# Optimization experiments

Measured on AMD Instinct MI355X. Metric: run time of the kernel, lower is better.

The kernel has to match this reference:

```python
import jax, jax.numpy as jnp
import numpy as np
import math

EMBED_DIMS = 256
NUM_LANDMARKS = 40  # hard-coded k=40 in the original module
B, N = 2, 8192


def setup_inputs() -> dict:
    key = jax.random.key(0)
    ks = jax.random.split(key, 9)
    C = EMBED_DIMS
    w = lambda k: jax.random.normal(k, (C, C), dtype=jnp.float32) * 0.02
    b = lambda k: jax.random.normal(k, (C,), dtype=jnp.float32) * 0.02
    return {
        "query": jax.random.normal(ks[0], (B, N, C), dtype=jnp.float32),
        "Wq": w(ks[1]), "bq": b(ks[2]),
        "Wk": w(ks[3]), "bk": b(ks[4]),
        "Wv": w(ks[5]), "bv": b(ks[6]),
        "Wo": w(ks[7]), "bo": b(ks[8]),
    }


def reference(query, Wq, bq, Wk, bk, Wv, bv, Wo, bo):
    # key = value = identity = query (defaults in the original forward)
    C = query.shape[-1]
    scaling = math.sqrt(C)

    q = query @ Wq.T + bq  # [B, N, C]
    k = query @ Wk.T + bk
    v = query @ Wv.T + bv

    # Full similarity only to score keys: score_m[b, m] = sum_n sim_nm[b, n, m]
    sim_nm = jnp.einsum('bnc,bmc->bnm', q, k) / scaling  # [B, N, N]
    score_m = sim_nm.sum(axis=1)                          # [B, N]

    _, top_idx = jax.lax.top_k(score_m, NUM_LANDMARKS)    # [B, 40]
    selected = jnp.take_along_axis(k, top_idx[:, :, None], axis=1)  # [B, 40, C]

    sim_qn = jax.nn.softmax(jnp.einsum('bnc,bkc->bnk', q, selected) / scaling, axis=-1)  # [B, N, 40]
    sim_km = jax.nn.softmax(jnp.einsum('bmc,bkc->bmk', k, selected) / scaling, axis=-1)  # [B, N, 40]

    sim_qk = jnp.einsum('bnk,bmk->bnm', sim_qn, sim_km)   # [B, N, N]
    out = jnp.einsum('bnm,bmc->bnc', sim_qk, v)           # [B, N, C]
    out = out @ Wo.T + bo
    return query + out  # identity residual; dropouts are identity at p=0
```

## Files before the change

kernel.cpp:

```cpp
#include <hip/hip_runtime.h>
#include <cstddef>
#include <cstdint>

#define BATCH 2
#define SEQ 8192
#define CH 256
#define NLM 40
#define NLMP 48
#define MROWS (BATCH * SEQ)
#define INV_SCALE 0.0625f
#define NCBLK 256

typedef unsigned short ushort_t;
typedef __attribute__((ext_vector_type(8))) short short8;
typedef __attribute__((ext_vector_type(4))) float floatx4;

__device__ __forceinline__ ushort_t f2bf(float f) {
    unsigned int u = __float_as_uint(f);
    u += 0x7FFFu + ((u >> 16) & 1u);
    return (ushort_t)(u >> 16);
}
__device__ __forceinline__ float bf2f(ushort_t u) {
    return __uint_as_float(((unsigned)u) << 16);
}

__device__ __forceinline__ void gload_lds16(const ushort_t* g, ushort_t* l) {
    __builtin_amdgcn_global_load_lds(
        (const __attribute__((address_space(1))) unsigned int*)g,
        (__attribute__((address_space(3))) unsigned int*)l, 16, 0, 0);
}

__global__ __launch_bounds__(256) void convert_colsum(const float* __restrict__ x,
                                                      ushort_t* __restrict__ xbf,
                                                      float* __restrict__ partial) {
    __shared__ float red[4][256];
    const int b = blockIdx.y;
    const int r0 = blockIdx.x * 32;
    const int t = threadIdx.x;
    const int c4 = (t & 63) * 4;
    const int rg = t >> 6;
    const float* base = x + ((size_t)b * SEQ + r0) * 256;
    ushort_t* obase = xbf + ((size_t)b * SEQ + r0) * 256;
    float4 s = {0.f, 0.f, 0.f, 0.f};
#pragma unroll
    for (int i = 0; i < 8; i++) {
        const int r = rg + i * 4;
        const float4 a = *(const float4*)&base[(size_t)r * 256 + c4];
        uint2 o;
        o.x = f2bf(a.x) | ((unsigned)f2bf(a.y) << 16);
        o.y = f2bf(a.z) | ((unsigned)f2bf(a.w) << 16);
        *(uint2*)&obase[(size_t)r * 256 + c4] = o;
        s.x += a.x; s.y += a.y; s.z += a.z; s.w += a.w;
    }
    *(float4*)&red[rg][c4] = s;
    __syncthreads();
    const float tot = red[0][t] + red[1][t] + red[2][t] + red[3][t];
    partial[((size_t)b * NCBLK + blockIdx.x) * 256 + t] = tot;
}

__global__ __launch_bounds__(1024) void ws_kernel(const float* __restrict__ partial,
                                                  const float* __restrict__ Wq,
                                                  const float* __restrict__ bq,
                                                  const float* __restrict__ Wk,
                                                  float* __restrict__ ws,
                                                  float* __restrict__ tmat) {
    const int b = blockIdx.x;
    __shared__ float xs[256];
    __shared__ float qs[256];
    __shared__ float ppart[4][256];
    const int t = threadIdx.x;
    {
        float* tz = tmat + (size_t)b * NLM * 256;
        for (int i = t; i < NLM * 256; i += 1024) tz[i] = 0.f;
    }
    {
        const int c = t & 255, qd = t >> 8;
        const float* pb = partial + ((size_t)b * NCBLK + qd * 64) * 256 + c;
        float a = 0.f;
#pragma unroll 8
        for (int i = 0; i < 64; i++) a += pb[(size_t)i * 256];
        ppart[qd][c] = a;
    }
    __syncthreads();
    if (t < 256) xs[t] = ppart[0][t] + ppart[1][t] + ppart[2][t] + ppart[3][t];
    __syncthreads();
    const int lane = t & 63, w = t >> 6;
    {
        float4 wq[16];
#pragma unroll
        for (int g = 0; g < 16; g++)
            wq[g] = *(const float4*)&Wq[(size_t)(w * 16 + g) * 256 + lane * 4];
        const float4 x4 = *(const float4*)&xs[lane * 4];
#pragma unroll
        for (int g = 0; g < 16; g++) {
            const int o = w * 16 + g;
            float d = wq[g].x * x4.x + wq[g].y * x4.y + wq[g].z * x4.z + wq[g].w * x4.w;
#pragma unroll
            for (int off = 32; off >= 1; off >>= 1) d += __shfl_down(d, off);
            if (lane == 0) qs[o] = d + 8192.0f * bq[o];
        }
    }
    __syncthreads();
    const int c = t & 255, part = t >> 8;
    float a = 0.f;
#pragma unroll 16
    for (int o = part * 64; o < part * 64 + 64; o++)
        a += Wk[(size_t)o * 256 + c] * qs[o];
    ppart[part][c] = a;
    __syncthreads();
    if (t < 256)
        ws[b * 256 + t] = ppart[0][t] + ppart[1][t] + ppart[2][t] + ppart[3][t];
}

__global__ __launch_bounds__(256) void gemm_qkv_score(const ushort_t* __restrict__ xbf,
                                                      const float* __restrict__ Wq,
                                                      const float* __restrict__ Wk,
                                                      const float* __restrict__ Wv,
                                                      const float* __restrict__ bq,
                                                      const float* __restrict__ bk,
                                                      const float* __restrict__ bv,
                                                      ushort_t* __restrict__ qkv,
                                                      const float* __restrict__ query,
                                                      const float* __restrict__ ws,
                                                      float* __restrict__ score) {
    __shared__ __align__(16) char smem[24576];
    ushort_t* As = (ushort_t*)smem;
    ushort_t* Bs = (ushort_t*)(smem + 16384);
    ushort_t* Es = (ushort_t*)smem;
    const int lin = blockIdx.x;
    const int wg = (lin & 7) * 256 + (lin >> 3);
    const int bx = wg & 3;
    const int by = (wg >> 2) & 127;
    const int z = wg >> 9;
    const int t = threadIdx.x;
    const int lane = t & 63;
    const int w = t >> 6;

    if (z == 3) {
        const int blk = by * 4 + bx;
#pragma unroll
        for (int i = 0; i < 8; i++) {
            const int g = blk * 32 + i * 4 + w;
            const int b = g >> 13;
            const int m = g & 8191;
            const float4 kv = *(const float4*)&query[(size_t)g * 256 + lane * 4];
            const float4 qs = *(const float4*)&ws[b * 256 + lane * 4];
            float d = kv.x * qs.x + kv.y * qs.y + kv.z * qs.z + kv.w * qs.w;
#pragma unroll
            for (int off = 32; off >= 1; off >>= 1) d += __shfl_down(d, off);
            if (lane == 0) score[(size_t)b * SEQ + m] = d * INV_SCALE;
        }
        return;
    }

    const float* __restrict__ W = (z == 0) ? Wq : (z == 1) ? Wk : Wv;
    const float* __restrict__ bias = (z == 0) ? bq : (z == 1) ? bk : bv;
    ushort_t* __restrict__ out = qkv + (size_t)z * MROWS * 256;
    const int o0 = bx * 64;
    const int m0 = by * 128;
    const int quad = lane >> 4;
    const int l16 = lane & 15;
    const int xsw = l16 & 7;

    floatx4 acc[2][4];
#pragma unroll
    for (int rt = 0; rt < 2; rt++)
#pragma unroll
        for (int ct = 0; ct < 4; ct++) acc[rt][ct] = (floatx4){0.f, 0.f, 0.f, 0.f};

    for (int kc = 0; kc < 256; kc += 64) {
#pragma unroll
        for (int q = 0; q < 4; q++) {
            const int r0 = w * 32 + q * 8;
            gload_lds16(&xbf[(size_t)(m0 + r0 + (lane >> 3)) * 256 + kc +
                             (((lane & 7) ^ (lane >> 3)) * 8)],
                        &As[r0 * 64]);
        }
#pragma unroll
        for (int u = 0; u < 2; u++) {
            const int cid = t + u * 256;
            const int row = cid >> 3;
            const int cch = cid & 7;
            const float* wp = &W[(size_t)(o0 + row) * 256 + kc + cch * 8];
            const float4 a = *(const float4*)wp;
            const float4 c = *(const float4*)(wp + 4);
            uint4 o;
            o.x = f2bf(a.x) | ((unsigned)f2bf(a.y) << 16);
            o.y = f2bf(a.z) | ((unsigned)f2bf(a.w) << 16);
            o.z = f2bf(c.x) | ((unsigned)f2bf(c.y) << 16);
            o.w = f2bf(c.z) | ((unsigned)f2bf(c.w) << 16);
            *(uint4*)&Bs[row * 64 + ((cch ^ (row & 7)) * 8)] = o;
        }
        __syncthreads();
#pragma unroll
        for (int s = 0; s < 2; s++) {
            short8 a[2], bf[4];
#pragma unroll
            for (int rt = 0; rt < 2; rt++)
                a[rt] = *(const short8*)&As[(w * 32 + rt * 16 + l16) * 64 +
                                            (((s * 4 + quad) ^ xsw) * 8)];
#pragma unroll
            for (int ct = 0; ct < 4; ct++)
                bf[ct] = *(const short8*)&Bs[(ct * 16 + l16) * 64 +
                                             (((s * 4 + quad) ^ xsw) * 8)];
#pragma unroll
            for (int rt = 0; rt < 2; rt++)
#pragma unroll
                for (int ct = 0; ct < 4; ct++)
                    acc[rt][ct] = __builtin_amdgcn_mfma_f32_16x16x32_bf16(
                        a[rt], bf[ct], acc[rt][ct], 0, 0, 0);
        }
        __syncthreads();
    }

#pragma unroll
    for (int rt = 0; rt < 2; rt++) {
#pragma unroll
        for (int ct = 0; ct < 4; ct++) {
            const int col = ct * 16 + l16;
            const float bb = bias[o0 + col];
#pragma unroll
            for (int reg = 0; reg < 4; reg++) {
                const int row = w * 32 + rt * 16 + quad * 4 + reg;
                Es[row * 72 + col] = f2bf(acc[rt][ct][reg] + bb);
            }
        }
    }
    __syncthreads();
#pragma unroll
    for (int u = 0; u < 4; u++) {
        const int cid = t + u * 256;
        const int row = cid >> 3;
        const int off = (cid & 7) * 8;
        *(uint4*)&out[(size_t)(m0 + row) * 256 + o0 + off] =
            *(const uint4*)&Es[row * 72 + off];
    }
}

__global__ __launch_bounds__(1024) void topk_gather(const float* __restrict__ score,
                                                    const ushort_t* __restrict__ kmat,
                                                    ushort_t* __restrict__ sel) {
    const int b = blockIdx.x;
    const int t = threadIdx.x;
    __shared__ unsigned hist[256];
    __shared__ unsigned wsum[64];
    __shared__ unsigned sPrefix, sMask, sRem, sNeq;
    __shared__ int sNgt;
    __shared__ int top[NLM];
    __shared__ unsigned topkey[NLM];

    unsigned key[8];
#pragma unroll
    for (int j = 0; j < 8; j++) {
        const unsigned u = __float_as_uint(score[(size_t)b * SEQ + t + j * 1024]);
        key[j] = u ^ (unsigned)(((int)u >> 31) | 0x80000000);
    }
    if (t == 0) { sPrefix = 0; sMask = 0; sRem = NLM; sNgt = 0; sNeq = 0; }

    for (int lvl = 0; lvl < 4; lvl++) {
        const int shift = 24 - 8 * lvl;
        if (t < 256) hist[t] = 0;
        __syncthreads();
        const unsigned pfx = sPrefix, msk = sMask;
#pragma unroll
        for (int j = 0; j < 8; j++)
            if (((key[j] ^ pfx) & msk) == 0)
                atomicAdd(&hist[(key[j] >> shift) & 255u], 1u);
        __syncthreads();
        if (t < 64) wsum[t] = hist[t * 4] + hist[t * 4 + 1] + hist[t * 4 + 2] + hist[t * 4 + 3];
        __syncthreads();
        if (t == 0) {
            unsigned rem = sRem, cum = 0;
            int g = 63;
            for (; g > 0; g--) { if (cum + wsum[g] >= rem) break; cum += wsum[g]; }
            int d = g * 4 + 3;
            for (; d > g * 4; d--) { if (cum + hist[d] >= rem) break; cum += hist[d]; }
            sRem = rem - cum;
            sPrefix |= ((unsigned)d) << shift;
            sMask |= 255u << shift;
        }
        __syncthreads();
    }
    const unsigned K40 = sPrefix;
    const unsigned rem = sRem;
    const int ngt = NLM - (int)rem;

#pragma unroll
    for (int j = 0; j < 8; j++) {
        if (key[j] > K40) {
            const int slot = atomicAdd(&sNgt, 1);
            top[slot] = t + j * 1024; topkey[slot] = key[j];
        } else if (key[j] == K40) {
            const unsigned e = atomicAdd(&sNeq, 1u);
            if (e < rem) {
                const int slot = ngt + (int)e;
                top[slot] = t + j * 1024; topkey[slot] = key[j];
            }
        }
    }
    __syncthreads();

    if (t < 64) {
        unsigned long long c = (t < NLM)
            ? ((((unsigned long long)(~topkey[t])) << 32) | (unsigned)top[t])
            : 0xFFFFFFFFFFFFFFFFull;
#pragma unroll
        for (int kk = 2; kk <= 64; kk <<= 1) {
#pragma unroll
            for (int j = kk >> 1; j >= 1; j >>= 1) {
                const unsigned long long o = __shfl_xor(c, j);
                const bool takeMin = ((t & kk) == 0) == ((t & j) == 0);
                const bool less = c < o;
                c = (takeMin == less) ? c : o;
            }
        }
        if (t < NLM) top[t] = (int)(c & 0xFFFFFFFFu);
    }
    __syncthreads();

    for (int f = t; f < NLMP * 256; f += 1024) {
        const int j = f >> 8;
        const int cc = f & 255;
        sel[(size_t)b * NLMP * 256 + f] =
            (j < NLM) ? kmat[((size_t)b * SEQ + top[j]) * 256 + cc] : (ushort_t)0;
    }
}

__global__ __launch_bounds__(256, 4) void sim_fused(const ushort_t* __restrict__ qbf,
                                                    const ushort_t* __restrict__ kbf,
                                                    const ushort_t* __restrict__ vbf,
                                                    const ushort_t* __restrict__ sel,
                                                    float* __restrict__ simq,
                                                    float* __restrict__ tmat) {
    __shared__ __align__(16) char smem[43008];
    float (*Ps)[40]  = (float(*)[40])smem;
    ushort_t* Vs     = (ushort_t*)(smem + 10240);
    const int b = blockIdx.y;
    const int n0 = blockIdx.x * 64;
    const int t = threadIdx.x;
    const int lane = t & 63;
    const int w = t >> 6;
    const int quad = lane >> 4;
    const int l16 = lane & 15;
    const ushort_t* __restrict__ A = (blockIdx.z == 0) ? qbf : kbf;
    const ushort_t* __restrict__ Arow = A + ((size_t)b * SEQ + n0 + w * 16 + l16) * 256;
    const ushort_t* __restrict__ Sb = sel + (size_t)b * NLMP * 256 + (size_t)l16 * 256;

    floatx4 acc[3];
#pragma unroll
    for (int ct = 0; ct < 3; ct++) acc[ct] = (floatx4){0.f, 0.f, 0.f, 0.f};

#pragma unroll
    for (int ks = 0; ks < 8; ks++) {
        const int ko = ks * 32 + quad * 8;
        const short8 a  = *(const short8*)&Arow[ko];
        const short8 b0 = *(const short8*)&Sb[ko];
        const short8 b1 = *(const short8*)&Sb[16 * 256 + ko];
        const short8 b2 = *(const short8*)&Sb[32 * 256 + ko];
        acc[0] = __builtin_amdgcn_mfma_f32_16x16x32_bf16(a, b0, acc[0], 0, 0, 0);
        acc[1] = __builtin_amdgcn_mfma_f32_16x16x32_bf16(a, b1, acc[1], 0, 0, 0);
        acc[2] = __builtin_amdgcn_mfma_f32_16x16x32_bf16(a, b2, acc[2], 0, 0, 0);
    }

    const bool v2ok = (l16 < 8);
    float p0[4], p1[4], p2[4];
#pragma unroll
    for (int reg = 0; reg < 4; reg++) {
        const float l0 = acc[0][reg] * INV_SCALE;
        const float l1 = acc[1][reg] * INV_SCALE;
        const float l2 = acc[2][reg] * INV_SCALE;
        float m = fmaxf(l0, l1);
        if (v2ok) m = fmaxf(m, l2);
        m = fmaxf(m, __shfl_xor(m, 1));
        m = fmaxf(m, __shfl_xor(m, 2));
        m = fmaxf(m, __shfl_xor(m, 4));
        m = fmaxf(m, __shfl_xor(m, 8));
        const float e0 = expf(l0 - m);
        const float e1 = expf(l1 - m);
        const float e2 = v2ok ? expf(l2 - m) : 0.f;
        float s = e0 + e1 + e2;
        s += __shfl_xor(s, 1);
        s += __shfl_xor(s, 2);
        s += __shfl_xor(s, 4);
        s += __shfl_xor(s, 8);
        const float inv = 1.f / s;
        p0[reg] = e0 * inv; p1[reg] = e1 * inv; p2[reg] = e2 * inv;
    }

    const int row0 = w * 16 + quad * 4;
    if (blockIdx.z == 0) {
        float* __restrict__ dst = &simq[((size_t)b * SEQ + n0 + row0) * NLM];
#pragma unroll
        for (int reg = 0; reg < 4; reg++) {
            float* __restrict__ d2 = dst + reg * NLM;
            d2[l16] = p0[reg];
            d2[16 + l16] = p1[reg];
            if (v2ok) d2[32 + l16] = p2[reg];
        }
        return;
    }

#pragma unroll
    for (int reg = 0; reg < 4; reg++) {
        Ps[row0 + reg][l16] = p0[reg];
        Ps[row0 + reg][16 + l16] = p1[reg];
        if (v2ok) Ps[row0 + reg][32 + l16] = p2[reg];
    }
#pragma unroll
    for (int u = 0; u < 8; u++) {
        gload_lds16(&vbf[((size_t)b * SEQ + n0 + w * 2 + u * 8 + (lane >> 5)) * 256 +
                         (lane & 31) * 8],
                    &Vs[(w * 2 + u * 8) * 256]);
    }
    __syncthreads();

    float tac[40];
#pragma unroll
    for (int j = 0; j < 40; j++) tac[j] = 0.f;

#pragma unroll 2
    for (int m = 0; m < 64; m++) {
        const float vv = bf2f(Vs[m * 256 + t]);
#pragma unroll
        for (int j4 = 0; j4 < 10; j4++) {
            const float4 p = *(const float4*)&Ps[m][j4 * 4];
            tac[j4 * 4 + 0] = fmaf(p.x, vv, tac[j4 * 4 + 0]);
            tac[j4 * 4 + 1] = fmaf(p.y, vv, tac[j4 * 4 + 1]);
            tac[j4 * 4 + 2] = fmaf(p.z, vv, tac[j4 * 4 + 2]);
            tac[j4 * 4 + 3] = fmaf(p.w, vv, tac[j4 * 4 + 3]);
        }
    }
#pragma unroll
    for (int j = 0; j < 40; j++)
        atomicAdd(&tmat[(size_t)b * NLM * 256 + j * 256 + t], tac[j]);
}

__global__ __launch_bounds__(512) void out_fused(const float* __restrict__ simq,
                                                 const float* __restrict__ tmat,
                                                 const float* __restrict__ Wo,
                                                 const float* __restrict__ bias,
                                                 const float* __restrict__ resid,
                                                 float* __restrict__ out) {
    __shared__ __align__(16) char smem[51200];
    float* Ps = (float*)smem;
    ushort_t* Ac = (ushort_t*)(smem + 10240);
    ushort_t* Bs = (ushort_t*)(smem + 18432);

    const int t = threadIdx.x;
    const int m0 = blockIdx.x * 64;
    const int b = blockIdx.x >> 7;
    const int lane = t & 63;
    const int w = t >> 6;
    const int quad = lane >> 4;
    const int l16 = lane & 15;
    const int xsw = l16 & 7;
    const int rt_base = (w & 3) * 16;
    const int cg_base = (w >> 2) * 8;

    for (int f = t; f < 64 * NLM; f += 512)
        Ps[f] = simq[(size_t)m0 * NLM + f];
    __syncthreads();

    floatx4 acc[8];
#pragma unroll
    for (int ct = 0; ct < 8; ct++) acc[ct] = (floatx4){0.f, 0.f, 0.f, 0.f};

    const int kl = t & 63;
    const int rg = t >> 6;
    const float* __restrict__ Tb = tmat + (size_t)b * NLM * 256;

    for (int kc = 0; kc < 256; kc += 64) {
        {
            float tc[40];
#pragma unroll
            for (int l = 0; l < 40; l++) tc[l] = Tb[l * 256 + kc + kl];
#pragma unroll
            for (int r = rg * 8; r < rg * 8 + 8; r++) {
                float a = 0.f;
#pragma unroll
                for (int j4 = 0; j4 < 10; j4++) {
                    const float4 p = *(const float4*)&Ps[r * 40 + j4 * 4];
                    a = fmaf(p.x, tc[j4 * 4 + 0], a);
                    a = fmaf(p.y, tc[j4 * 4 + 1], a);
                    a = fmaf(p.z, tc[j4 * 4 + 2], a);
                    a = fmaf(p.w, tc[j4 * 4 + 3], a);
                }
                Ac[r * 64 + (((kl >> 3) ^ (r & 7)) * 8) + (kl & 7)] = f2bf(a);
            }
        }
#pragma unroll
        for (int u = 0; u < 4; u++) {
            const int cid = t + u * 512;
            const int row = cid >> 3;
            const int cch = cid & 7;
            const float* wp = &Wo[(size_t)row * 256 + kc + cch * 8];
            const float4 a = *(const float4*)wp;
            const float4 c = *(const float4*)(wp + 4);
            uint4 o;
            o.x = f2bf(a.x) | ((unsigned)f2bf(a.y) << 16);
            o.y = f2bf(a.z) | ((unsigned)f2bf(a.w) << 16);
            o.z = f2bf(c.x) | ((unsigned)f2bf(c.y) << 16);
            o.w = f2bf(c.z) | ((unsigned)f2bf(c.w) << 16);
            *(uint4*)&Bs[row * 64 + ((cch ^ (row & 7)) * 8)] = o;
        }
        __syncthreads();
#pragma unroll
        for (int s = 0; s < 2; s++) {
            const short8 a = *(const short8*)&Ac[(rt_base + l16) * 64 +
                                                 (((s * 4 + quad) ^ xsw) * 8)];
#pragma unroll
            for (int ct = 0; ct < 8; ct++) {
                const short8 bf = *(const short8*)&Bs[((cg_base + ct) * 16 + l16) * 64 +
                                                      (((s * 4 + quad) ^ xsw) * 8)];
                acc[ct] = __builtin_amdgcn_mfma_f32_16x16x32_bf16(a, bf, acc[ct], 0, 0, 0);
            }
        }
        __syncthreads();
    }

#pragma unroll
    for (int ct = 0; ct < 8; ct++) {
        const int col = (cg_base + ct) * 16 + l16;
        const float bb = bias[col];
#pragma unroll
        for (int reg = 0; reg < 4; reg++) {
            const int row = rt_base + quad * 4 + reg;
            const size_t idx = (size_t)(m0 + row) * 256 + col;
            out[idx] = (acc[ct][reg] + bb) + resid[idx];
        }
    }
}

extern "C" void kernel_launch(void* const* d_in, const int* in_sizes, int n_in,
                              void* d_out, int out_size, void* d_ws, size_t ws_size,
                              hipStream_t stream) {
    const float* query = (const float*)d_in[0];
    const float* Wq = (const float*)d_in[1];
    const float* bq = (const float*)d_in[2];
    const float* Wk = (const float*)d_in[3];
    const float* bk = (const float*)d_in[4];
    const float* Wv = (const float*)d_in[5];
    const float* bv = (const float*)d_in[6];
    const float* Wo = (const float*)d_in[7];
    const float* bo = (const float*)d_in[8];
    float* out = (float*)d_out;

    char* p = (char*)d_ws;
    float* simq  = (float*)p;            p += (size_t)MROWS * NLM * 4;
    ushort_t* selbf = (ushort_t*)p;      p += (size_t)BATCH * NLMP * 256 * 2;
    float* tmat  = (float*)p;            p += (size_t)BATCH * NLM * 256 * 4;
    float* partial = (float*)p;          p += (size_t)BATCH * NCBLK * 256 * 4;
    float* ws    = (float*)p;            p += (size_t)BATCH * 256 * 4;
    float* score = (float*)p;            p += (size_t)BATCH * SEQ * 4;
    ushort_t* qkv = (ushort_t*)p;        p += (size_t)3 * MROWS * 256 * 2;
    ushort_t* xbf = (ushort_t*)p;        p += (size_t)MROWS * 256 * 2;
    ushort_t* qbf = qkv;
    ushort_t* kbf = qkv + (size_t)MROWS * 256;
    ushort_t* vbf = qkv + (size_t)2 * MROWS * 256;

    const dim3 blk(256);

    convert_colsum<<<dim3(SEQ / 32, BATCH), blk, 0, stream>>>(query, xbf, partial);
    ws_kernel<<<dim3(BATCH), dim3(1024), 0, stream>>>(partial, Wq, bq, Wk, ws, tmat);

    gemm_qkv_score<<<dim3(2048), blk, 0, stream>>>(
        xbf, Wq, Wk, Wv, bq, bk, bv, qkv, query, ws, score);

    topk_gather<<<dim3(BATCH), dim3(1024), 0, stream>>>(score, kbf, selbf);

    sim_fused<<<dim3(SEQ / 64, BATCH, 2), blk, 0, stream>>>(qbf, kbf, vbf, selbf, simq, tmat);

    out_fused<<<dim3(MROWS / 64), dim3(512), 0, stream>>>(simq, tmat, Wo, bo, query, out);
}
```

Measured before the change: 185.2 us.

## Precompute full P·T tile once in out_fused and parallelize top-k digit search

Result: faster. 175.3 us, median of 2 (-5.3%).

```diff
diff --git a/kernel.cpp b/kernel.cpp
--- a/kernel.cpp
+++ b/kernel.cpp
@@ -243,7 +243,6 @@
     const int b = blockIdx.x;
     const int t = threadIdx.x;
     __shared__ unsigned hist[256];
-    __shared__ unsigned wsum[64];
     __shared__ unsigned sPrefix, sMask, sRem, sNeq;
     __shared__ int sNgt;
     __shared__ int top[NLM];
@@ -267,17 +266,26 @@
             if (((key[j] ^ pfx) & msk) == 0)
                 atomicAdd(&hist[(key[j] >> shift) & 255u], 1u);
         __syncthreads();
-        if (t < 64) wsum[t] = hist[t * 4] + hist[t * 4 + 1] + hist[t * 4 + 2] + hist[t * 4 + 3];
-        __syncthreads();
-        if (t == 0) {
-            unsigned rem = sRem, cum = 0;
-            int g = 63;
-            for (; g > 0; g--) { if (cum + wsum[g] >= rem) break; cum += wsum[g]; }
-            int d = g * 4 + 3;
-            for (; d > g * 4; d--) { if (cum + hist[d] >= rem) break; cum += hist[d]; }
-            sRem = rem - cum;
-            sPrefix |= ((unsigned)d) << shift;
-            sMask |= 255u << shift;
+        if (t < 64) {
+            unsigned sfx = hist[t * 4] + hist[t * 4 + 1] + hist[t * 4 + 2] + hist[t * 4 + 3];
+#pragma unroll
+            for (int off = 1; off < 64; off <<= 1) {
+                const unsigned o = __shfl_down(sfx, off);
+                if (t + off < 64) sfx += o;
+            }
+            const unsigned rem = sRem;
+            const unsigned long long mk = __ballot(sfx >= rem);
+            const int gstar = 63 - __builtin_clzll(mk);
+            unsigned S1 = __shfl(sfx, (gstar + 1) & 63);
+            if (gstar == 63) S1 = 0u;
+            if (t == 0) {
+                int d = gstar * 4 + 3;
+                unsigned cum = S1;
+                for (; d > gstar * 4; d--) { if (cum + hist[d] >= rem) break; cum += hist[d]; }
+                sRem = rem - cum;
+                sPrefix |= ((unsigned)d) << shift;
+                sMask |= 255u << shift;
+            }
         }
         __syncthreads();
     }
@@ -441,10 +449,10 @@
                                                  const float* __restrict__ bias,
                                                  const float* __restrict__ resid,
                                                  float* __restrict__ out) {
-    __shared__ __align__(16) char smem[51200];
+    __shared__ __align__(16) char smem[75776];
     float* Ps = (float*)smem;
     ushort_t* Ac = (ushort_t*)(smem + 10240);
-    ushort_t* Bs = (ushort_t*)(smem + 18432);
+    ushort_t* Bs = (ushort_t*)(smem + 43008);
 
     const int t = threadIdx.x;
     const int m0 = blockIdx.x * 64;
@@ -461,33 +469,36 @@
         Ps[f] = simq[(size_t)m0 * NLM + f];
     __syncthreads();
 
+    {
+        const int col = t & 255;
+        const int r0 = (t >> 8) * 32;
+        const float* __restrict__ Tb = tmat + (size_t)b * NLM * 256;
+        float tc[40];
+#pragma unroll
+        for (int l = 0; l < 40; l++) tc[l] = Tb[l * 256 + col];
+        const int chunk = col >> 3;
+#pragma unroll
+        for (int r = 0; r < 32; r++) {
+            const int rr = r0 + r;
+            float a = 0.f;
+#pragma unroll
+            for (int j4 = 0; j4 < 10; j4++) {
+                const float4 p = *(const float4*)&Ps[rr * 40 + j4 * 4];
+                a = fmaf(p.x, tc[j4 * 4 + 0], a);
+                a = fmaf(p.y, tc[j4 * 4 + 1], a);
+                a = fmaf(p.z, tc[j4 * 4 + 2], a);
+                a = fmaf(p.w, tc[j4 * 4 + 3], a);
+            }
+            const int pch = (chunk & ~7) | ((chunk & 7) ^ (rr & 7));
+            Ac[rr * 256 + pch * 8 + (col & 7)] = f2bf(a);
+        }
+    }
+
     floatx4 acc[8];
 #pragma unroll
     for (int ct = 0; ct < 8; ct++) acc[ct] = (floatx4){0.f, 0.f, 0.f, 0.f};
 
-    const int kl = t & 63;
-    const int rg = t >> 6;
-    const float* __restrict__ Tb = tmat + (size_t)b * NLM * 256;
-
     for (int kc = 0; kc < 256; kc += 64) {
-        {
-            float tc[40];
-#pragma unroll
-            for (int l = 0; l < 40; l++) tc[l] = Tb[l * 256 + kc + kl];
-#pragma unroll
-            for (int r = rg * 8; r < rg * 8 + 8; r++) {
-                float a = 0.f;
-#pragma unroll
-                for (int j4 = 0; j4 < 10; j4++) {
-                    const float4 p = *(const float4*)&Ps[r * 40 + j4 * 4];
-                    a = fmaf(p.x, tc[j4 * 4 + 0], a);
-                    a = fmaf(p.y, tc[j4 * 4 + 1], a);
-                    a = fmaf(p.z, tc[j4 * 4 + 2], a);
-                    a = fmaf(p.w, tc[j4 * 4 + 3], a);
-                }
-                Ac[r * 64 + (((kl >> 3) ^ (r & 7)) * 8) + (kl & 7)] = f2bf(a);
-            }
-        }
 #pragma unroll
         for (int u = 0; u < 4; u++) {
             const int cid = t + u * 512;
@@ -506,8 +517,8 @@
         __syncthreads();
 #pragma unroll
         for (int s = 0; s < 2; s++) {
-            const short8 a = *(const short8*)&Ac[(rt_base + l16) * 64 +
-                                                 (((s * 4 + quad) ^ xsw) * 8)];
+            const short8 a = *(const short8*)&Ac[(rt_base + l16) * 256 +
+                                                 ((kc >> 3) + ((s * 4 + quad) ^ xsw)) * 8];
 #pragma unroll
             for (int ct = 0; ct < 8; ct++) {
                 const short8 bf = *(const short8*)&Bs[((cg_base + ct) * 16 + l16) * 64 +
```
